# Kernel tuning notes

Measured on AMD Instinct MI355X. Metric: run time of the kernel, lower is better.

## Reference

```python
import jax, jax.numpy as jnp
import numpy as np

HEAD_DIM = 64
NUM_HEAD = 8
NUM_CLUSTERS = 16
B, N, M = 2, 2048, 2048


def setup_inputs() -> dict:
    key = jax.random.key(0)
    ks = jax.random.split(key, 10)
    d = HEAD_DIM
    inp = {
        "Q": jax.random.normal(ks[0], (B, NUM_HEAD, N, d), jnp.float32),
        "K": jax.random.normal(ks[1], (B, NUM_HEAD, M, d), jnp.float32),
        "V": jax.random.normal(ks[2], (B, NUM_HEAD, M, d), jnp.float32),
        "mask": jnp.zeros((B, M), jnp.int32),
        "noise": jax.random.uniform(ks[3], (B, NUM_HEAD, N, M), jnp.float32),
        "emb": jax.random.normal(ks[4], (NUM_HEAD * NUM_CLUSTERS, d), jnp.float32),
        "W1": jax.random.normal(ks[5], (d, d), jnp.float32) * 0.02,
        "b1": jnp.zeros((d,), jnp.float32),
        "W2": jax.random.normal(ks[6], (d, d), jnp.float32) * 0.02,
        "b2": jnp.zeros((d,), jnp.float32),
        "W3": jax.random.normal(ks[7], (d, d), jnp.float32) * 0.02,
        "b3": jnp.zeros((d,), jnp.float32),
    }
    return inp


def _proj(x, W1, b1, W2, b2, W3, b3):
    # torch nn.Linear: y = x @ W.T + b; dropout is identity in eval mode
    x = jax.nn.relu(jnp.einsum("bhnd,ed->bhne", x, W1) + b1)
    x = jax.nn.relu(jnp.einsum("bhnd,ed->bhne", x, W2) + b2)
    return jnp.einsum("bhnd,ed->bhne", x, W3) + b3


def reference(Q, K, V, mask, noise, emb, W1, b1, W2, b2, W3, b3):
    b, h, n, d = Q.shape
    m = V.shape[2]
    k = NUM_CLUSTERS

    clusters = emb.reshape(h, k, d)                                  # [h,k,d]
    dist = jnp.einsum("hkd,hjd->hkj", clusters, clusters)            # [h,k,k]
    # softmax over the flattened k*k matrix per head
    S = jax.nn.softmax(dist.reshape(h, k * k), axis=-1).reshape(h, k, k)

    Qhat = jax.nn.sigmoid(jnp.einsum("bhnd,hkd->bhnk", _proj(Q, W1, b1, W2, b2, W3, b3), clusters))
    Khat = jax.nn.sigmoid(jnp.einsum("bhmd,hkd->bhmk", _proj(K, W1, b1, W2, b2, W3, b3), clusters))

    SK = jnp.einsum("hkj,bhmj->bhkm", S, Khat)                       # [b,h,k,m]
    expA = jnp.einsum("bhnk,bhkm->bhnm", Qhat, SK)                   # Bernoulli probs in [0,1]

    # SampleGraphSparseGraph: Bernoulli sample with straight-through gradient
    sample = (noise < expA).astype(Q.dtype)
    graph = expA + jax.lax.stop_gradient(sample - expA)

    dot = jnp.einsum("bhnd,bhmd->bhnm", Q, K) / jnp.sqrt(jnp.asarray(d, Q.dtype))
    dot = jnp.where(mask[:, None, None, :] == 1, -jnp.inf, dot)
    p = jax.nn.softmax(dot, axis=-1) * graph
    # F.normalize(p=1): x / max(||x||_1, 1e-12); p is non-negative
    attn = p / jnp.maximum(jnp.sum(p, axis=-1, keepdims=True), 1e-12)

    X = jnp.einsum("bhnm,bhmd->bhnd", attn, V)
    sparsity = jnp.sum(graph, axis=(0, -1, -2)) / (b * n * m)        # [h]
    return X, sparsity, graph, attn
```

## Files before the change

### kernel.cpp

```cpp
#include <hip/hip_runtime.h>


typedef float  f32x4 __attribute__((ext_vector_type(4)));
typedef float  f32x8 __attribute__((ext_vector_type(8)));
typedef double f64x2 __attribute__((ext_vector_type(2)));
typedef __bf16 bf16x8 __attribute__((ext_vector_type(8)));

__device__ __forceinline__ unsigned short f2bf(float f) {
  __bf16 b = (__bf16)f;
  return __builtin_bit_cast(unsigned short, b);
}
__device__ __forceinline__ float bf2f(unsigned short u) {
  return (float)__builtin_bit_cast(__bf16, u);
}

__global__ __launch_bounds__(256) void kS(const float* __restrict__ emb,
                                          double* __restrict__ wsS,
                                          float* __restrict__ wsSP) {
  __shared__ double c[16][65];
  __shared__ double red[256];
  const int t = threadIdx.x, h = blockIdx.x;
  if (t == 0) wsSP[h] = 0.f;
  for (int i = t; i < 1024; i += 256) c[i >> 6][i & 63] = (double)emb[(size_t)h * 1024 + i];
  __syncthreads();
  const int k = t >> 4, j = t & 15;
  double acc = 0.0;
  for (int d = 0; d < 64; ++d) acc += c[k][d] * c[j][d];
  red[t] = acc; __syncthreads();
  for (int s = 128; s > 0; s >>= 1) { if (t < s) red[t] = fmax(red[t], red[t + s]); __syncthreads(); }
  const double mx = red[0]; __syncthreads();
  const double e = exp(acc - mx);
  red[t] = e; __syncthreads();
  for (int s = 128; s > 0; s >>= 1) { if (t < s) red[t] += red[t + s]; __syncthreads(); }
  wsS[h * 256 + t] = e / red[0];
}

__global__ __launch_bounds__(256) void kMLP(
    const float* __restrict__ Q, const float* __restrict__ K,
    const float* __restrict__ emb,
    const float* __restrict__ W1, const float* __restrict__ b1,
    const float* __restrict__ W2, const float* __restrict__ b2,
    const float* __restrict__ W3, const float* __restrict__ b3,
    const double* __restrict__ wsS,
    double* __restrict__ QHAT, double* __restrict__ SKT) {
  __shared__ double Xt[64][66];
  __shared__ float  Wl[64][68];
  __shared__ float  bsS[64];
  __shared__ float  cl[16][68];
  __shared__ double kh[64][17];
  __shared__ double Sl[256];

  const int t = threadIdx.x;
  const int blk = blockIdx.x;
  const int side = blk >> 9;
  const int idx = blk & 511;
  const int bh = idx >> 5;
  const int h = bh & 7;
  const int chunk = idx & 31;
  const size_t t0 = (size_t)bh * 2048 + (size_t)chunk * 64;

  const float* src = side ? K : Q;
  for (int i = t; i < 4096; i += 256) Xt[i >> 6][i & 63] = (double)src[t0 * 64 + i];

  const float* Ws[3] = {W1, W2, W3};
  const float* bs[3] = {b1, b2, b3};
  const int te = t & 15, tt = t >> 4;
  const int e0 = te * 4, tok0 = tt * 4;

  for (int l = 0; l < 3; ++l) {
    __syncthreads();
    for (int i = t; i < 4096; i += 256) Wl[i >> 6][i & 63] = Ws[l][i];
    if (t < 64) bsS[t] = bs[l][t];
    __syncthreads();
    double o[4][4];
#pragma unroll
    for (int i = 0; i < 4; ++i)
#pragma unroll
      for (int j = 0; j < 4; ++j) o[i][j] = 0.0;
    for (int d = 0; d < 64; d += 4) {
      double xa[4][4];
#pragma unroll
      for (int i = 0; i < 4; ++i) {
        const f64x2 lo = *(const f64x2*)&Xt[tok0 + i][d];
        const f64x2 hi = *(const f64x2*)&Xt[tok0 + i][d + 2];
        xa[i][0] = lo[0]; xa[i][1] = lo[1]; xa[i][2] = hi[0]; xa[i][3] = hi[1];
      }
      float4 wb[4];
#pragma unroll
      for (int j = 0; j < 4; ++j) wb[j] = *(const float4*)&Wl[e0 + j][d];
#pragma unroll
      for (int dd = 0; dd < 4; ++dd) {
        const double w0 = (double)((dd == 0) ? wb[0].x : (dd == 1) ? wb[0].y : (dd == 2) ? wb[0].z : wb[0].w);
        const double w1 = (double)((dd == 0) ? wb[1].x : (dd == 1) ? wb[1].y : (dd == 2) ? wb[1].z : wb[1].w);
        const double w2 = (double)((dd == 0) ? wb[2].x : (dd == 1) ? wb[2].y : (dd == 2) ? wb[2].z : wb[2].w);
        const double w3 = (double)((dd == 0) ? wb[3].x : (dd == 1) ? wb[3].y : (dd == 2) ? wb[3].z : wb[3].w);
#pragma unroll
        for (int i = 0; i < 4; ++i) {
          const double xv = xa[i][dd];
          o[i][0] += xv * w0; o[i][1] += xv * w1; o[i][2] += xv * w2; o[i][3] += xv * w3;
        }
      }
    }
#pragma unroll
    for (int i = 0; i < 4; ++i)
#pragma unroll
      for (int j = 0; j < 4; ++j) {
        double v = o[i][j] + (double)bsS[e0 + j];
        if (l < 2) v = fmax(v, 0.0);
        o[i][j] = v;
      }
    __syncthreads();
#pragma unroll
    for (int i = 0; i < 4; ++i)
#pragma unroll
      for (int j = 0; j < 4; ++j) Xt[tok0 + i][e0 + j] = o[i][j];
  }
  __syncthreads();
  for (int i = t; i < 1024; i += 256) cl[i >> 6][i & 63] = emb[(size_t)h * 1024 + i];
  if (side) { for (int i = t; i < 256; i += 256) Sl[i] = wsS[h * 256 + i]; }
  __syncthreads();

  const int tok = t >> 2, k0 = (t & 3) * 4;
  double z[4] = {0.0, 0.0, 0.0, 0.0};
  for (int d = 0; d < 64; d += 2) {
    const f64x2 xv = *(const f64x2*)&Xt[tok][d];
    const float2 c0 = *(const float2*)&cl[k0 + 0][d];
    const float2 c1 = *(const float2*)&cl[k0 + 1][d];
    const float2 c2 = *(const float2*)&cl[k0 + 2][d];
    const float2 c3 = *(const float2*)&cl[k0 + 3][d];
    z[0] += xv[0] * (double)c0.x; z[1] += xv[0] * (double)c1.x;
    z[2] += xv[0] * (double)c2.x; z[3] += xv[0] * (double)c3.x;
    z[0] += xv[1] * (double)c0.y; z[1] += xv[1] * (double)c1.y;
    z[2] += xv[1] * (double)c2.y; z[3] += xv[1] * (double)c3.y;
  }
  double hat[4];
#pragma unroll
  for (int j = 0; j < 4; ++j) hat[j] = 1.0 / (1.0 + exp(-z[j]));

  if (!side) {
#pragma unroll
    for (int j = 0; j < 4; ++j) QHAT[(t0 + tok) * 16 + k0 + j] = hat[j];
  } else {
    kh[tok][k0 + 0] = hat[0]; kh[tok][k0 + 1] = hat[1];
    kh[tok][k0 + 2] = hat[2]; kh[tok][k0 + 3] = hat[3];
    __syncthreads();
    double sk[4] = {0.0, 0.0, 0.0, 0.0};
    for (int jj = 0; jj < 16; ++jj) {
      const double kv = kh[tok][jj];
      sk[0] += Sl[(k0 + 0) * 16 + jj] * kv; sk[1] += Sl[(k0 + 1) * 16 + jj] * kv;
      sk[2] += Sl[(k0 + 2) * 16 + jj] * kv; sk[3] += Sl[(k0 + 3) * 16 + jj] * kv;
    }
#pragma unroll
    for (int j = 0; j < 4; ++j) SKT[(t0 + tok) * 16 + k0 + j] = sk[j];
  }
}

__global__ __launch_bounds__(256) void kSample(
    const float* __restrict__ noise,
    const double* __restrict__ qhat, const double* __restrict__ skt,
    float* __restrict__ wsSP,
    unsigned long long* __restrict__ GB64, float* __restrict__ GOUT) {
  const int t = threadIdx.x;
  const int lane = t & 63, wave = t >> 6;
  const int nt = blockIdx.x;
  const int mt = blockIdx.y;
  const int bh = blockIdx.z, h = bh & 7;
  const int n0 = nt * 64;
  const int mA = mt * 512 + wave * 64 + lane;
  const int mB = mA + 256;

  double skvA[16], skvB[16];
  {
    const double* spA = skt + ((size_t)bh * 2048 + mA) * 16;
    const double* spB = skt + ((size_t)bh * 2048 + mB) * 16;
#pragma unroll
    for (int q = 0; q < 8; ++q) {
      *(f64x2*)(skvA + 2 * q) = *(const f64x2*)(spA + 2 * q);
      *(f64x2*)(skvB + 2 * q) = *(const f64x2*)(spB + 2 * q);
    }
  }

  const double* qbase = qhat + ((size_t)bh * 2048 + n0) * 16;
  const float* nzbase = noise + ((size_t)bh * 2048 + n0) * 2048;
  float* gobase = GOUT + ((size_t)bh * 2048 + n0) * 2048;
  unsigned long long* gbbase = GB64 + ((size_t)bh * 2048 + n0) * 32;
  const int gA = mA >> 6, gB = mB >> 6;

  int cnt = 0;
  for (int n = 0; n < 64; ++n) {
    const double* qr = qbase + (size_t)n * 16;
    double ea0 = 0.0, ea1 = 0.0;
#pragma unroll
    for (int k = 0; k < 16; ++k) {
      const double qk = qr[k];
      ea0 += qk * skvA[k];
      ea1 += qk * skvB[k];
    }
    const float nzA = nzbase[(size_t)n * 2048 + mA];
    const float nzB = nzbase[(size_t)n * 2048 + mB];
    const int g0 = ((double)nzA < ea0) ? 1 : 0;
    const int g1 = ((double)nzB < ea1) ? 1 : 0;
    cnt += g0 + g1;
    const unsigned long long b0 = __ballot(g0);
    const unsigned long long b1 = __ballot(g1);
    if (lane == 0) {
      gbbase[(size_t)n * 32 + gA] = b0;
      gbbase[(size_t)n * 32 + gB] = b1;
    }
    gobase[(size_t)n * 2048 + mA] = g0 ? 1.0f : 0.0f;
    gobase[(size_t)n * 2048 + mB] = g1 ? 1.0f : 0.0f;
  }
  cnt += __shfl_xor(cnt, 1); cnt += __shfl_xor(cnt, 2); cnt += __shfl_xor(cnt, 4);
  cnt += __shfl_xor(cnt, 8); cnt += __shfl_xor(cnt, 16); cnt += __shfl_xor(cnt, 32);
  if (lane == 0) atomicAdd(&wsSP[h], (float)cnt);
}

__global__ __launch_bounds__(256) void kCvt(const float* __restrict__ K,
                                            const float* __restrict__ V,
                                            unsigned short* __restrict__ KB,
                                            unsigned short* __restrict__ VT) {
  __shared__ float vt[128][65];
  const int t = threadIdx.x;
  const int bh = blockIdx.x, ch = blockIdx.y;
  const size_t base = ((size_t)bh * 2048 + ch * 128) * 64;
  for (int i = t; i < 8192; i += 256) {
    KB[base + i] = f2bf(K[base + i]);
    vt[i >> 6][i & 63] = V[base + i];
  }
  __syncthreads();
  const size_t vbase = (size_t)bh * 64 * 2048 + ch * 128;
  for (int i = t; i < 8192; i += 256) {
    const int d = i >> 7, mm = i & 127;
    VT[vbase + (size_t)d * 2048 + mm] = f2bf(vt[mm][d]);
  }
}

__global__ __launch_bounds__(256, 2) void kAttn(
    const float* __restrict__ Q, const int* __restrict__ maskp,
    const unsigned short* __restrict__ KB, const unsigned short* __restrict__ VT,
    const unsigned int* __restrict__ GB32,
    float* __restrict__ XOUT, float* __restrict__ AOUT) {
  __shared__ unsigned int bitsS[16][64];
  __shared__ unsigned short stageS[4][16][32];
  __shared__ float dredS[4][16];
  __shared__ float dinvS[16];
  __shared__ float xredS[16][68];

  const int t = threadIdx.x;
  const int wave = t >> 6, lane = t & 63;
  const int bh = blockIdx.y, b = bh >> 3;
  const int n0 = blockIdx.x * 16;
  const int hi2 = lane >> 4;
  const int hi8 = hi2 << 3;
  const int g4 = hi2 << 2;
  const int lm = lane & 15;

  for (int i = t; i < 1024; i += 256)
    bitsS[i >> 6][i & 63] = GB32[((size_t)bh * 2048 + n0 + (i >> 6)) * 64 + (i & 63)];
  for (int i = t; i < 16 * 68; i += 256) ((float*)xredS)[i] = 0.f;

  const float* qrow = Q + ((size_t)bh * 2048 + n0 + lm) * 64;
  bf16x8 aq[2];
#pragma unroll
  for (int hh = 0; hh < 2; ++hh) {
    const int d0 = hi8 + hh * 32;
    const f32x4 qa = *(const f32x4*)(qrow + d0);
    const f32x4 qb = *(const f32x4*)(qrow + d0 + 4);
    bf16x8 v;
    v[0] = (__bf16)qa[0]; v[1] = (__bf16)qa[1]; v[2] = (__bf16)qa[2]; v[3] = (__bf16)qa[3];
    v[4] = (__bf16)qb[0]; v[5] = (__bf16)qb[1]; v[6] = (__bf16)qb[2]; v[7] = (__bf16)qb[3];
    aq[hh] = v;
  }

  const unsigned short* kbp = KB + (size_t)bh * 2048 * 64;
  const unsigned short* vtp = VT + (size_t)bh * 64 * 2048;
  const int* mkp = maskp + b * 2048;
  __syncthreads();

  float dsum[4] = {0.f, 0.f, 0.f, 0.f};
  f32x4 xacc[4];
#pragma unroll
  for (int td = 0; td < 4; ++td) xacc[td] = (f32x4){0.f, 0.f, 0.f, 0.f};
  unsigned int upk[64];

#pragma unroll
  for (int it = 0; it < 16; ++it) {
    const int mb = (wave << 9) + (it << 5);
    f32x4 st[2];
#pragma unroll
    for (int tt = 0; tt < 2; ++tt) {
      const unsigned short* kr = kbp + (size_t)(mb + tt * 16 + lm) * 64 + hi8;
      const bf16x8 b0 = *(const bf16x8*)(kr);
      const bf16x8 b1 = *(const bf16x8*)(kr + 32);
      f32x4 acc = (f32x4){0.f, 0.f, 0.f, 0.f};
      acc = __builtin_amdgcn_mfma_f32_16x16x32_bf16(aq[0], b0, acc, 0, 0, 0);
      acc = __builtin_amdgcn_mfma_f32_16x16x32_bf16(aq[1], b1, acc, 0, 0, 0);
      st[tt] = acc;
    }
#pragma unroll
    for (int tt = 0; tt < 2; ++tt) {
      const int mv = mkp[mb + tt * 16 + lm];
      const f32x4 sv4 = st[tt];
#pragma unroll
      for (int r = 0; r < 4; ++r) {
        const int row = g4 + r;
        const int g = (bitsS[row][mb >> 5] >> (tt * 16 + lm)) & 1;
        const float u = (g && !mv) ? __expf(sv4[r] * 0.125f) : 0.f;
        dsum[r] += u;
        const unsigned short ub = f2bf(u);
        const int slot = it * 4 + tt * 2 + (r >> 1);
        if (r & 1) upk[slot] |= ((unsigned int)ub) << 16;
        else       upk[slot] = (unsigned int)ub;
        stageS[wave][row][(tt * 16 + lm) ^ (((row >> 2) & 3) << 3)] = ub;
      }
    }
    {
      const int rdcol = hi8 ^ (((lm >> 2) & 3) << 3);
      const bf16x8 ua = *(const bf16x8*)&stageS[wave][lm][rdcol];
#pragma unroll
      for (int td = 0; td < 4; ++td) {
        const bf16x8 vb = *(const bf16x8*)(vtp + (size_t)(td * 16 + lm) * 2048 + mb + hi8);
        xacc[td] = __builtin_amdgcn_mfma_f32_16x16x32_bf16(ua, vb, xacc[td], 0, 0, 0);
      }
    }
  }

#pragma unroll
  for (int r = 0; r < 4; ++r) {
    float v = dsum[r];
    v += __shfl_xor(v, 1); v += __shfl_xor(v, 2); v += __shfl_xor(v, 4); v += __shfl_xor(v, 8);
    if (lm == 0) dredS[wave][g4 + r] = v;
  }
  __syncthreads();
  if (t < 16) {
    const float dv = dredS[0][t] + dredS[1][t] + dredS[2][t] + dredS[3][t];
    dinvS[t] = 1.0f / fmaxf(dv, 1e-12f);
  }
  __syncthreads();

  const size_t rowbase = (size_t)bh * 2048 + n0;
#pragma unroll
  for (int it = 0; it < 16; ++it) {
    const int mb = (wave << 9) + (it << 5);
#pragma unroll
    for (int tt = 0; tt < 2; ++tt)
#pragma unroll
      for (int r = 0; r < 4; ++r) {
        const int row = g4 + r;
        const int slot = it * 4 + tt * 2 + (r >> 1);
        const unsigned short ub =
            (r & 1) ? (unsigned short)(upk[slot] >> 16) : (unsigned short)(upk[slot] & 0xFFFF);
        stageS[wave][row][(tt * 16 + lm) ^ (((row >> 2) & 3) << 3)] = ub;
      }
    const int row = lane >> 2, q = lane & 3;
    const int rc = (q * 8) ^ (((row >> 2) & 3) << 3);
    const unsigned short* up = &stageS[wave][row][rc];
    const float inv = dinvS[row];
    f32x8 av;
#pragma unroll
    for (int j = 0; j < 8; ++j) av[j] = bf2f(up[j]) * inv;
    *(f32x8*)(AOUT + (rowbase + row) * 2048 + mb + q * 8) = av;
  }

  for (int w = 0; w < 4; ++w) {
    if (wave == w) {
#pragma unroll
      for (int td = 0; td < 4; ++td)
#pragma unroll
        for (int r = 0; r < 4; ++r) xredS[g4 + r][td * 16 + lm] += xacc[td][r];
    }
    __syncthreads();
  }
  for (int i = t; i < 1024; i += 256) {
    const int nl = i >> 6, d = i & 63;
    XOUT[(rowbase + nl) * 64 + d] = xredS[nl][d] * dinvS[nl];
  }
}

__global__ void kFin(const float* __restrict__ wsSP, float* __restrict__ SPOUT) {
  const int t = threadIdx.x;
  if (t < 8) SPOUT[t] = wsSP[t] * (1.0f / 8388608.0f);
}

extern "C" void kernel_launch(void* const* d_in, const int* in_sizes, int n_in,
                              void* d_out, int out_size, void* d_ws, size_t ws_size,
                              hipStream_t stream) {
  const float* Q = (const float*)d_in[0];
  const float* K = (const float*)d_in[1];
  const float* V = (const float*)d_in[2];
  const int* mask = (const int*)d_in[3];
  const float* noise = (const float*)d_in[4];
  const float* emb = (const float*)d_in[5];
  const float* W1 = (const float*)d_in[6];
  const float* b1 = (const float*)d_in[7];
  const float* W2 = (const float*)d_in[8];
  const float* b2 = (const float*)d_in[9];
  const float* W3 = (const float*)d_in[10];
  const float* b3 = (const float*)d_in[11];

  char* ws = (char*)d_ws;
  double* wsS = (double*)(ws + 0);
  float* wsSP = (float*)(ws + 16384);
  double* QHAT = (double*)(ws + 32768);
  double* SKT  = (double*)(ws + 32768 + 4194304);
  unsigned short* KB = (unsigned short*)(ws + 32768);
  unsigned short* VT = (unsigned short*)(ws + 32768 + 4194304);
  unsigned long long* GB64 = (unsigned long long*)(ws + 32768 + 8388608);
  unsigned int* GB32 = (unsigned int*)(ws + 32768 + 8388608);

  float* out = (float*)d_out;
  float* XOUT = out;
  float* SPOUT = out + 2097152;
  float* GOUT = out + 2097160;
  float* AOUT = out + 69206024;

  kS<<<8, 256, 0, stream>>>(emb, wsS, wsSP);
  kMLP<<<1024, 256, 0, stream>>>(Q, K, emb, W1, b1, W2, b2, W3, b3, wsS, QHAT, SKT);
  kSample<<<dim3(32, 4, 16), 256, 0, stream>>>(noise, QHAT, SKT, wsSP, GB64, GOUT);
  kCvt<<<dim3(16, 16), 256, 0, stream>>>(K, V, KB, VT);
  kAttn<<<dim3(128, 16), 256, 0, stream>>>(Q, mask, KB, VT, GB32, XOUT, AOUT);
  kFin<<<1, 64, 0, stream>>>(wsSP, SPOUT);
}
```

Before: 546.4 us.

## Recompute QK scores in a second pass instead of caching packed probabilities in registers

The attention kernel no longer holds 64 registers of packed bf16 probabilities between the row-sum pass and the output pass. The first pass now only accumulates the masked exponential sums. The second pass recomputes the QK MFMA and exponentials, does the PV MFMA, and writes the normalized attention rows. With the register array gone, launch bounds rise from 2 to 4 blocks per CU to raise occupancy. The cost is running the K loads, QK MFMAs and exps twice, and the loops are no longer forced to unroll.

After: 506.7 us. 7.3% less time.

```diff
diff --git a/kernel.cpp b/kernel.cpp
--- a/kernel.cpp
+++ b/kernel.cpp
@@ -235,7 +235,7 @@
   }
 }
 
-__global__ __launch_bounds__(256, 2) void kAttn(
+__global__ __launch_bounds__(256, 4) void kAttn(
     const float* __restrict__ Q, const int* __restrict__ maskp,
     const unsigned short* __restrict__ KB, const unsigned short* __restrict__ VT,
     const unsigned int* __restrict__ GB32,
@@ -278,12 +278,6 @@
   __syncthreads();
 
   float dsum[4] = {0.f, 0.f, 0.f, 0.f};
-  f32x4 xacc[4];
-#pragma unroll
-  for (int td = 0; td < 4; ++td) xacc[td] = (f32x4){0.f, 0.f, 0.f, 0.f};
-  unsigned int upk[64];
-
-#pragma unroll
   for (int it = 0; it < 16; ++it) {
     const int mb = (wave << 9) + (it << 5);
     f32x4 st[2];
@@ -303,28 +297,11 @@
       const f32x4 sv4 = st[tt];
 #pragma unroll
       for (int r = 0; r < 4; ++r) {
-        const int row = g4 + r;
-        const int g = (bitsS[row][mb >> 5] >> (tt * 16 + lm)) & 1;
-        const float u = (g && !mv) ? __expf(sv4[r] * 0.125f) : 0.f;
-        dsum[r] += u;
-        const unsigned short ub = f2bf(u);
-        const int slot = it * 4 + tt * 2 + (r >> 1);
-        if (r & 1) upk[slot] |= ((unsigned int)ub) << 16;
-        else       upk[slot] = (unsigned int)ub;
-        stageS[wave][row][(tt * 16 + lm) ^ (((row >> 2) & 3) << 3)] = ub;
-      }
-    }
-    {
-      const int rdcol = hi8 ^ (((lm >> 2) & 3) << 3);
-      const bf16x8 ua = *(const bf16x8*)&stageS[wave][lm][rdcol];
-#pragma unroll
-      for (int td = 0; td < 4; ++td) {
-        const bf16x8 vb = *(const bf16x8*)(vtp + (size_t)(td * 16 + lm) * 2048 + mb + hi8);
-        xacc[td] = __builtin_amdgcn_mfma_f32_16x16x32_bf16(ua, vb, xacc[td], 0, 0, 0);
-      }
-    }
-  }
-
+        const int g = (bitsS[g4 + r][mb >> 5] >> (tt * 16 + lm)) & 1;
+        if (g && !mv) dsum[r] += __expf(sv4[r] * 0.125f);
+      }
+    }
+  }
 #pragma unroll
   for (int r = 0; r < 4; ++r) {
     float v = dsum[r];
@@ -339,27 +316,55 @@
   __syncthreads();
 
   const size_t rowbase = (size_t)bh * 2048 + n0;
-#pragma unroll
+  f32x4 xacc[4];
+#pragma unroll
+  for (int td = 0; td < 4; ++td) xacc[td] = (f32x4){0.f, 0.f, 0.f, 0.f};
+
   for (int it = 0; it < 16; ++it) {
     const int mb = (wave << 9) + (it << 5);
-#pragma unroll
-    for (int tt = 0; tt < 2; ++tt)
+    f32x4 st[2];
+#pragma unroll
+    for (int tt = 0; tt < 2; ++tt) {
+      const unsigned short* kr = kbp + (size_t)(mb + tt * 16 + lm) * 64 + hi8;
+      const bf16x8 b0 = *(const bf16x8*)(kr);
+      const bf16x8 b1 = *(const bf16x8*)(kr + 32);
+      f32x4 acc = (f32x4){0.f, 0.f, 0.f, 0.f};
+      acc = __builtin_amdgcn_mfma_f32_16x16x32_bf16(aq[0], b0, acc, 0, 0, 0);
+      acc = __builtin_amdgcn_mfma_f32_16x16x32_bf16(aq[1], b1, acc, 0, 0, 0);
+      st[tt] = acc;
+    }
+#pragma unroll
+    for (int tt = 0; tt < 2; ++tt) {
+      const int mv = mkp[mb + tt * 16 + lm];
+      const f32x4 sv4 = st[tt];
 #pragma unroll
       for (int r = 0; r < 4; ++r) {
         const int row = g4 + r;
-        const int slot = it * 4 + tt * 2 + (r >> 1);
-        const unsigned short ub =
-            (r & 1) ? (unsigned short)(upk[slot] >> 16) : (unsigned short)(upk[slot] & 0xFFFF);
-        stageS[wave][row][(tt * 16 + lm) ^ (((row >> 2) & 3) << 3)] = ub;
-      }
-    const int row = lane >> 2, q = lane & 3;
-    const int rc = (q * 8) ^ (((row >> 2) & 3) << 3);
-    const unsigned short* up = &stageS[wave][row][rc];
-    const float inv = dinvS[row];
-    f32x8 av;
-#pragma unroll
-    for (int j = 0; j < 8; ++j) av[j] = bf2f(up[j]) * inv;
-    *(f32x8*)(AOUT + (rowbase + row) * 2048 + mb + q * 8) = av;
+        const int g = (bitsS[row][mb >> 5] >> (tt * 16 + lm)) & 1;
+        const float u = (g && !mv) ? __expf(sv4[r] * 0.125f) : 0.f;
+        const int col = tt * 16 + lm;
+        stageS[wave][row][col ^ (((row >> 2) & 3) << 3)] = f2bf(u);
+      }
+    }
+    {
+      const int rdcol = hi8 ^ (((lm >> 2) & 3) << 3);
+      const bf16x8 ua = *(const bf16x8*)&stageS[wave][lm][rdcol];
+#pragma unroll
+      for (int td = 0; td < 4; ++td) {
+        const bf16x8 vb = *(const bf16x8*)(vtp + (size_t)(td * 16 + lm) * 2048 + mb + hi8);
+        xacc[td] = __builtin_amdgcn_mfma_f32_16x16x32_bf16(ua, vb, xacc[td], 0, 0, 0);
+      }
+    }
+    {
+      const int row = lane >> 2, q = lane & 3;
+      const int rc = (q * 8) ^ (((row >> 2) & 3) << 3);
+      const unsigned short* up = &stageS[wave][row][rc];
+      const float inv = dinvS[row];
+      f32x8 av;
+#pragma unroll
+      for (int j = 0; j < 8; ++j) av[j] = bf2f(up[j]) * inv;
+      *(f32x8*)(AOUT + (rowbase + row) * 2048 + mb + q * 8) = av;
+    }
   }
 
   for (int w = 0; w < 4; ++w) {
```
